# Kernel tuning notes

Hardware: AMD Instinct MI355X
Metric: run time of the kernel (lower is better)

Reference implementation:

```python
import jax, jax.numpy as jnp
import numpy as np
import math

C = 1.0                      # curvature (default in __call__)
SQRT_C = 1.0
MIN_ENORM = 1e-15
PROJ_EPS = 1e-5              # ball boundary margin for proj
CLAMPING_FACTOR = 1.0
SMOOTHING_FACTOR = 50.0
EPS32 = float(np.finfo(np.float32).eps)
CLAMP = CLAMPING_FACTOR * float(math.log(2.0 / EPS32))   # ~16.64


def proj(x, c=C):
    """Project points onto the Poincare ball of curvature c."""
    norm = jnp.linalg.norm(x, axis=-1, keepdims=True).clip(min=MIN_ENORM)
    max_norm = (1.0 - PROJ_EPS) / jnp.sqrt(c)
    return x * jnp.where(norm > max_norm, max_norm / norm, 1.0)


def conformal_factor(x, c=C):
    # lambda_x = 2 / (1 - c * ||x||^2), keepdims
    return 2.0 / (1.0 - c * jnp.sum(x * x, axis=-1, keepdims=True))


def smooth_clamp(x, lo, hi, s):
    """Smooth clamp via scaled softplus: -> clamp(x, lo, hi) as s -> inf."""
    sp = lambda z: jax.nn.softplus(s * z) / s
    return lo + sp(x - lo) - sp(x - hi)


def setup_inputs() -> dict:
    key = jax.random.key(0)
    k1, k2, k3 = jax.random.split(key, 3)
    B, D, P = 8192, 128, 128
    # manifold points: scale into the ball then project
    x = proj(0.1 * jax.random.normal(k1, (B, D), dtype=jnp.float32))
    weight = jax.random.normal(k2, (P, D), dtype=jnp.float32)
    bias = 0.01 * jax.random.normal(k3, (P, D), dtype=jnp.float32)
    return {"x": x, "weight": weight, "bias": bias}


def reference(x, weight, bias):
    c, sqrt_c = C, SQRT_C
    # 0) project bias onto manifold: (P, D)
    bias_PD = proj(bias, c)
    # 1) parallel transport weight from origin to bias: u * (lambda_0 / lambda_p) = u * (1 - c||p||^2)
    pt_weight_PD = weight * (1.0 - c * jnp.sum(bias_PD * bias_PD, axis=-1, keepdims=True))
    a = pt_weight_PD                 # (P, D)
    p_neg = -bias_PD                 # (P, D)
    # pairwise Mobius addition (-p) (+) x  -> (P, B, D)
    x2 = jnp.sum(x * x, axis=-1)                 # (B,)
    p2 = jnp.sum(p_neg * p_neg, axis=-1)         # (P,)
    dot = jnp.einsum("pd,bd->pb", p_neg, x)     # (P, B)
    coef_p = 1.0 + 2.0 * c * dot + c * x2[None, :]          # (P, B)
    coef_x = 1.0 - c * p2[:, None]                            # (P, 1)
    den = 1.0 + 2.0 * c * dot + (c * c) * p2[:, None] * x2[None, :]  # (P, B)
    sub_PBD = (coef_p[:, :, None] * p_neg[:, None, :] + coef_x[:, :, None] * x[None, :, :]) / den[:, :, None]
    sub_BPD = jnp.transpose(sub_PBD, (1, 0, 2))  # (B, P, D)
    # <sub, a> and norms
    suba_BP = jnp.einsum("bpd,pd->bp", sub_BPD, a)
    a_norm_P = jnp.linalg.norm(a, axis=-1).clip(min=MIN_ENORM)   # (P,)
    lambda_sub_BP = 2.0 / (1.0 - c * jnp.sum(sub_BPD * sub_BPD, axis=-1))  # (B, P)
    asinh_arg_BP = sqrt_c * lambda_sub_BP * suba_BP / a_norm_P[None, :]
    asinh_arg_BP = smooth_clamp(asinh_arg_BP, -CLAMP, CLAMP, SMOOTHING_FACTOR)
    signed_dist_BP = jnp.arcsinh(asinh_arg_BP) / sqrt_c
    lambda_p_P = 2.0 / (1.0 - c * jnp.sum(bias_PD * bias_PD, axis=-1))     # (P,)
    res_BP = lambda_p_P[None, :] * a_norm_P[None, :] * signed_dist_BP
    return res_BP
```

## Files before the change

### kernel.cpp

```cpp
#include <hip/hip_runtime.h>
#include <math.h>

namespace {
constexpr int Bn = 8192, Pn = 128, Dn = 128;
constexpr int BT = 64, PT = 32;
constexpr float MAXN = 1.0f - 1e-5f;
constexpr float CLAMPV = 16.63553233343869f;
constexpr float SMOOTH = 50.0f;
}

typedef short bf8 __attribute__((ext_vector_type(8)));
typedef float f32x4 __attribute__((ext_vector_type(4)));

__device__ __forceinline__ unsigned short bf16rn(float f) {
  unsigned int u = __float_as_uint(f);
  u = u + 0x7fffu + ((u >> 16) & 1u);
  return (unsigned short)(u >> 16);
}
__device__ __forceinline__ float bf2f(unsigned short h) {
  return __uint_as_float(((unsigned int)h) << 16);
}
__device__ __forceinline__ void split3(float f, unsigned short& h,
                                       unsigned short& m, unsigned short& l) {
  h = bf16rn(f); float r1 = f - bf2f(h);
  m = bf16rn(r1); float r2 = r1 - bf2f(m);
  l = bf16rn(r2);
}

__global__ __launch_bounds__(512, 4)
void fused_kernel(const float* __restrict__ x,
                  const float* __restrict__ weight,
                  const float* __restrict__ bias,
                  float* __restrict__ out) {
  __shared__ float4 lds4[4608];
  __shared__ double psum[96];
  __shared__ float x2A[64], fbA[64];
  __shared__ float bwA[32], iaA[32], soA[32];

  float* const scpf = reinterpret_cast<float*>(lds4 + 3072);
  float* const scxf = reinterpret_cast<float*>(lds4 + 3072 + 768);
  ushort4* const ldsu4 = reinterpret_cast<ushort4*>(lds4);
  const bf8* const ldsb = reinterpret_cast<const bf8*>(lds4);

  const int tid = threadIdx.x;
  const int b0 = blockIdx.x * BT;
  const int p0 = blockIdx.y * PT;
  const int rr = tid >> 5;
  const int cc = tid & 31;

  float4 xv[4], wv[2], bv[2];
#pragma unroll
  for (int q = 0; q < 4; ++q)
    xv[q] = *reinterpret_cast<const float4*>(x + (size_t)(b0 + 16 * q + rr) * Dn + cc * 4);
#pragma unroll
  for (int q = 0; q < 2; ++q) {
    wv[q] = *reinterpret_cast<const float4*>(weight + (size_t)(p0 + 16 * q + rr) * Dn + cc * 4);
    bv[q] = *reinterpret_cast<const float4*>(bias + (size_t)(p0 + 16 * q + rr) * Dn + cc * 4);
  }

#pragma unroll
  for (int q = 0; q < 4; ++q) {
    const int r = 16 * q + rr;
    float4 v = xv[q];
    float a[4] = {v.x, v.y, v.z, v.w};
    unsigned short h[4], m[4], lo[4];
#pragma unroll
    for (int e = 0; e < 4; ++e) split3(a[e], h[e], m[e], lo[e]);
    const int base = ((r * 16 + ((cc >> 1) ^ (r & 15))) << 1) + (cc & 1);
    ldsu4[base]            = make_ushort4(h[0], h[1], h[2], h[3]);
    ldsu4[2048 + base]     = make_ushort4(m[0], m[1], m[2], m[3]);
    ldsu4[4096 + base]     = make_ushort4(lo[0], lo[1], lo[2], lo[3]);
    scxf[q * 512 + tid] = fmaf(a[0], a[0], fmaf(a[1], a[1], fmaf(a[2], a[2], a[3] * a[3])));
  }
#pragma unroll
  for (int q = 0; q < 2; ++q) {
    float4 w = wv[q], b = bv[q];
    scpf[(q * 3 + 0) * 512 + tid] = fmaf(b.x, b.x, fmaf(b.y, b.y, fmaf(b.z, b.z, b.w * b.w)));
    scpf[(q * 3 + 1) * 512 + tid] = fmaf(b.x, w.x, fmaf(b.y, w.y, fmaf(b.z, w.z, b.w * w.w)));
    scpf[(q * 3 + 2) * 512 + tid] = fmaf(w.x, w.x, fmaf(w.y, w.y, fmaf(w.z, w.z, w.w * w.w)));
  }
  __syncthreads();

  if (tid < 96) {
    const int row = tid / 3;
    const int val = tid - 3 * row;
    const float4* base = reinterpret_cast<const float4*>(scpf) +
                         ((row >> 4) * 3 + val) * 128 + (row & 15) * 8;
    double s = 0.0;
#pragma unroll
    for (int jj = 0; jj < 8; ++jj) {
      float4 f = base[(jj + tid) & 7];
      s += (double)f.x + (double)f.y + (double)f.z + (double)f.w;
    }
    psum[tid] = s;
  } else if (tid >= 256 && tid < 320) {
    const int r = tid - 256;
    const float4* base = reinterpret_cast<const float4*>(scxf) +
                         (r >> 4) * 128 + (r & 15) * 8;
    double s = 0.0;
#pragma unroll
    for (int jj = 0; jj < 8; ++jj) {
      float4 f = base[(jj + tid) & 7];
      s += (double)f.x + (double)f.y + (double)f.z + (double)f.w;
    }
    x2A[r] = (float)s;
    fbA[r] = (float)(2.0 / (1.0 - s));
  }
  __syncthreads();

#pragma unroll
  for (int q = 0; q < 2; ++q) {
    const int r = 16 * q + rr;
    double nb2 = psum[3 * r + 0];
    double bwd = psum[3 * r + 1];
    double w2  = psum[3 * r + 2];
    double norm = sqrt(nb2);
    if (norm < 1e-15) norm = 1e-15;
    double scl = (norm > (double)MAXN) ? (double)MAXN / norm : 1.0;
    double p2 = nb2 * scl * scl;
    const float cxf = (float)(1.0 - p2);
    const float bwf = (float)(scl * bwd);
    const float k2f = 2.0f * bwf * (float)scl;
    float4 w = wv[q], b = bv[q];
    float vvv[4];
    vvv[0] = fmaf(cxf, w.x, k2f * b.x);
    vvv[1] = fmaf(cxf, w.y, k2f * b.y);
    vvv[2] = fmaf(cxf, w.z, k2f * b.z);
    vvv[3] = fmaf(cxf, w.w, k2f * b.w);
    unsigned short h[4], m[4], lo[4];
#pragma unroll
    for (int e = 0; e < 4; ++e) split3(vvv[e], h[e], m[e], lo[e]);
    const int base = ((3072 + r * 16 + ((cc >> 1) ^ (r & 15))) << 1) + (cc & 1);
    ldsu4[base]        = make_ushort4(h[0], h[1], h[2], h[3]);
    ldsu4[1024 + base] = make_ushort4(m[0], m[1], m[2], m[3]);
    ldsu4[2048 + base] = make_ushort4(lo[0], lo[1], lo[2], lo[3]);
    if (cc == 0) {
      float an = cxf * sqrtf((float)w2);
      if (an < 1e-15f) an = 1e-15f;
      bwA[r] = bwf;
      iaA[r] = 1.0f / an;
      soA[r] = 2.0f / cxf * an;
    }
  }
  __syncthreads();

  const int wid = tid >> 6;
  const int l = tid & 63;
  const int strip = wid & 3;
  const int khalf = wid >> 2;
  const int arow = strip * 16 + (l & 15);
  const int prow0 = l & 15, prow1 = 16 + (l & 15);
  const int kgrp = l >> 4;
  f32x4 acc0 = {0.f, 0.f, 0.f, 0.f}, acc1 = {0.f, 0.f, 0.f, 0.f};
#pragma unroll
  for (int kc2 = 0; kc2 < 2; ++kc2) {
    const int ga = ((khalf * 2 + kc2) * 4 + kgrp) ^ (l & 15);
    bf8 aH = ldsb[0 * 1024 + arow * 16 + ga];
    bf8 aM = ldsb[1 * 1024 + arow * 16 + ga];
    bf8 aL = ldsb[2 * 1024 + arow * 16 + ga];
    bf8 b0H = ldsb[3072 + 0 * 512 + prow0 * 16 + ga];
    bf8 b0M = ldsb[3072 + 1 * 512 + prow0 * 16 + ga];
    bf8 b0L = ldsb[3072 + 2 * 512 + prow0 * 16 + ga];
    bf8 b1H = ldsb[3072 + 0 * 512 + prow1 * 16 + ga];
    bf8 b1M = ldsb[3072 + 1 * 512 + prow1 * 16 + ga];
    bf8 b1L = ldsb[3072 + 2 * 512 + prow1 * 16 + ga];
    acc0 = __builtin_amdgcn_mfma_f32_16x16x32_bf16(aL, b0H, acc0, 0, 0, 0);
    acc0 = __builtin_amdgcn_mfma_f32_16x16x32_bf16(aH, b0L, acc0, 0, 0, 0);
    acc0 = __builtin_amdgcn_mfma_f32_16x16x32_bf16(aM, b0M, acc0, 0, 0, 0);
    acc0 = __builtin_amdgcn_mfma_f32_16x16x32_bf16(aM, b0H, acc0, 0, 0, 0);
    acc0 = __builtin_amdgcn_mfma_f32_16x16x32_bf16(aH, b0M, acc0, 0, 0, 0);
    acc0 = __builtin_amdgcn_mfma_f32_16x16x32_bf16(aH, b0H, acc0, 0, 0, 0);
    acc1 = __builtin_amdgcn_mfma_f32_16x16x32_bf16(aL, b1H, acc1, 0, 0, 0);
    acc1 = __builtin_amdgcn_mfma_f32_16x16x32_bf16(aH, b1L, acc1, 0, 0, 0);
    acc1 = __builtin_amdgcn_mfma_f32_16x16x32_bf16(aM, b1M, acc1, 0, 0, 0);
    acc1 = __builtin_amdgcn_mfma_f32_16x16x32_bf16(aM, b1H, acc1, 0, 0, 0);
    acc1 = __builtin_amdgcn_mfma_f32_16x16x32_bf16(aH, b1M, acc1, 0, 0, 0);
    acc1 = __builtin_amdgcn_mfma_f32_16x16x32_bf16(aH, b1H, acc1, 0, 0, 0);
  }
  __syncthreads();

  lds4[khalf * 512 + strip * 128 + 0 * 64 + l] =
      make_float4(acc0[0], acc0[1], acc0[2], acc0[3]);
  lds4[khalf * 512 + strip * 128 + 1 * 64 + l] =
      make_float4(acc1[0], acc1[1], acc1[2], acc1[3]);
  __syncthreads();

  {
    const int es = tid >> 7;
    const int et = (tid >> 6) & 1;
    const int el = tid & 63;
    float4 pa = lds4[es * 128 + et * 64 + el];
    float4 pb = lds4[512 + es * 128 + et * 64 + el];
    float s4[4] = {pa.x + pb.x, pa.y + pb.y, pa.z + pb.z, pa.w + pb.w};
    const int pl = et * 16 + (el & 15);
    const float bwp = bwA[pl], iap = iaA[pl], sop = soA[pl];
#pragma unroll
    for (int reg = 0; reg < 4; ++reg) {
      const int brl = es * 16 + (el >> 4) * 4 + reg;
      const float x2i = x2A[brl];
      const float fbi = fbA[brl];
      float X = fmaf(-(1.0f + x2i), bwp, s4[reg]);
      float arg = X * fbi * iap;
      float aa = fabsf(arg);
      float argc;
      if (aa <= CLAMPV - 0.35f) {
        argc = aa;
      } else if (aa >= CLAMPV + 0.35f) {
        argc = CLAMPV;
      } else {
        float z = SMOOTH * (aa - CLAMPV);
        float sp = (fmaxf(z, 0.0f) + log1pf(__expf(-fabsf(z)))) * (1.0f / SMOOTH);
        argc = aa - sp;
      }
      float r = __logf(argc + sqrtf(fmaf(argc, argc, 1.0f)));
      out[(size_t)(b0 + brl) * Pn + p0 + pl] = copysignf(sop * r, arg);
    }
  }
}

extern "C" void kernel_launch(void* const* d_in, const int* in_sizes, int n_in,
                              void* d_out, int out_size, void* d_ws, size_t ws_size,
                              hipStream_t stream) {
  const float* x = (const float*)d_in[0];
  const float* w = (const float*)d_in[1];
  const float* bias = (const float*)d_in[2];
  float* out = (float*)d_out;

  hipLaunchKernelGGL(fused_kernel, dim3(Bn / BT, Pn / PT), dim3(512), 0, stream,
                     x, w, bias, out);
}
```

Before: 14.08 us.

## Split MFMA work by output tile instead of K halves to drop LDS reduction

Each of the 8 waves now owns a distinct 16x16 output tile (4 B-strips by 2 P-tiles) and runs the full K=128 loop, rather than pairs of waves each covering half of K and then combining partial sums through LDS. This removes a barrier plus the LDS store/load round trip for the partial accumulators, and the epilogue reads results straight from registers. Global loads are also regrouped so each thread handles 16 x-elements or 8 w/b-elements and writes 16-byte bf16 vectors to LDS. Partial norms are reduced in float per thread before the double-precision sum, which slightly changes the numerics.

```diff
diff --git a/kernel.cpp b/kernel.cpp
--- a/kernel.cpp
+++ b/kernel.cpp
@@ -10,6 +10,7 @@
 }
 
 typedef short bf8 __attribute__((ext_vector_type(8)));
+typedef unsigned short u16x8 __attribute__((ext_vector_type(8)));
 typedef float f32x4 __attribute__((ext_vector_type(4)));
 
 __device__ __forceinline__ unsigned short bf16rn(float f) {
@@ -37,83 +38,89 @@
   __shared__ float x2A[64], fbA[64];
   __shared__ float bwA[32], iaA[32], soA[32];
 
-  float* const scpf = reinterpret_cast<float*>(lds4 + 3072);
-  float* const scxf = reinterpret_cast<float*>(lds4 + 3072 + 768);
-  ushort4* const ldsu4 = reinterpret_cast<ushort4*>(lds4);
-  const bf8* const ldsb = reinterpret_cast<const bf8*>(lds4);
+  u16x8* const LU = reinterpret_cast<u16x8*>(lds4);
+  const bf8* const LB = reinterpret_cast<const bf8*>(lds4);
+  float* const scp = reinterpret_cast<float*>(lds4 + 3072);
+  float* const scx = scp + 1536;
 
   const int tid = threadIdx.x;
   const int b0 = blockIdx.x * BT;
   const int p0 = blockIdx.y * PT;
-  const int rr = tid >> 5;
-  const int cc = tid & 31;
-
-  float4 xv[4], wv[2], bv[2];
-#pragma unroll
-  for (int q = 0; q < 4; ++q)
-    xv[q] = *reinterpret_cast<const float4*>(x + (size_t)(b0 + 16 * q + rr) * Dn + cc * 4);
-#pragma unroll
-  for (int q = 0; q < 2; ++q) {
-    wv[q] = *reinterpret_cast<const float4*>(weight + (size_t)(p0 + 16 * q + rr) * Dn + cc * 4);
-    bv[q] = *reinterpret_cast<const float4*>(bias + (size_t)(p0 + 16 * q + rr) * Dn + cc * 4);
-  }
-
-#pragma unroll
-  for (int q = 0; q < 4; ++q) {
-    const int r = 16 * q + rr;
-    float4 v = xv[q];
-    float a[4] = {v.x, v.y, v.z, v.w};
-    unsigned short h[4], m[4], lo[4];
-#pragma unroll
-    for (int e = 0; e < 4; ++e) split3(a[e], h[e], m[e], lo[e]);
-    const int base = ((r * 16 + ((cc >> 1) ^ (r & 15))) << 1) + (cc & 1);
-    ldsu4[base]            = make_ushort4(h[0], h[1], h[2], h[3]);
-    ldsu4[2048 + base]     = make_ushort4(m[0], m[1], m[2], m[3]);
-    ldsu4[4096 + base]     = make_ushort4(lo[0], lo[1], lo[2], lo[3]);
-    scxf[q * 512 + tid] = fmaf(a[0], a[0], fmaf(a[1], a[1], fmaf(a[2], a[2], a[3] * a[3])));
-  }
-#pragma unroll
-  for (int q = 0; q < 2; ++q) {
-    float4 w = wv[q], b = bv[q];
-    scpf[(q * 3 + 0) * 512 + tid] = fmaf(b.x, b.x, fmaf(b.y, b.y, fmaf(b.z, b.z, b.w * b.w)));
-    scpf[(q * 3 + 1) * 512 + tid] = fmaf(b.x, w.x, fmaf(b.y, w.y, fmaf(b.z, w.z, b.w * w.w)));
-    scpf[(q * 3 + 2) * 512 + tid] = fmaf(w.x, w.x, fmaf(w.y, w.y, fmaf(w.z, w.z, w.w * w.w)));
+
+  const int rA = tid >> 3, sA = tid & 7;
+  {
+    float xe[16];
+    const float* xr = x + (size_t)(b0 + rA) * Dn + sA * 16;
+#pragma unroll
+    for (int j = 0; j < 4; ++j) {
+      float4 q = *reinterpret_cast<const float4*>(xr + 4 * j);
+      xe[4 * j] = q.x; xe[4 * j + 1] = q.y; xe[4 * j + 2] = q.z; xe[4 * j + 3] = q.w;
+    }
+    float s2 = 0.f;
+#pragma unroll
+    for (int e = 0; e < 16; ++e) s2 = fmaf(xe[e], xe[e], s2);
+    scx[sA * 64 + rA] = s2;
+    const int sw = rA & 15;
+#pragma unroll
+    for (int g = 0; g < 2; ++g) {
+      u16x8 H, M, L;
+#pragma unroll
+      for (int e = 0; e < 8; ++e) {
+        unsigned short h, m, l;
+        split3(xe[g * 8 + e], h, m, l);
+        H[e] = h; M[e] = m; L[e] = l;
+      }
+      const int slot = rA * 16 + ((2 * sA + g) ^ sw);
+      LU[slot] = H;
+      LU[1024 + slot] = M;
+      LU[2048 + slot] = L;
+    }
+  }
+  const int rP = tid >> 4, sP = tid & 15;
+  float we[8], be[8];
+  {
+    const float* wr = weight + (size_t)(p0 + rP) * Dn + sP * 8;
+    const float* br = bias + (size_t)(p0 + rP) * Dn + sP * 8;
+#pragma unroll
+    for (int j = 0; j < 2; ++j) {
+      float4 qw = *reinterpret_cast<const float4*>(wr + 4 * j);
+      float4 qb = *reinterpret_cast<const float4*>(br + 4 * j);
+      we[4 * j] = qw.x; we[4 * j + 1] = qw.y; we[4 * j + 2] = qw.z; we[4 * j + 3] = qw.w;
+      be[4 * j] = qb.x; be[4 * j + 1] = qb.y; be[4 * j + 2] = qb.z; be[4 * j + 3] = qb.w;
+    }
+    float nb2 = 0.f, bwd = 0.f, w2 = 0.f;
+#pragma unroll
+    for (int e = 0; e < 8; ++e) {
+      nb2 = fmaf(be[e], be[e], nb2);
+      bwd = fmaf(be[e], we[e], bwd);
+      w2  = fmaf(we[e], we[e], w2);
+    }
+    scp[0 * 512 + sP * 32 + rP] = nb2;
+    scp[1 * 512 + sP * 32 + rP] = bwd;
+    scp[2 * 512 + sP * 32 + rP] = w2;
   }
   __syncthreads();
 
   if (tid < 96) {
-    const int row = tid / 3;
-    const int val = tid - 3 * row;
-    const float4* base = reinterpret_cast<const float4*>(scpf) +
-                         ((row >> 4) * 3 + val) * 128 + (row & 15) * 8;
+    const int stat = tid >> 5, row = tid & 31;
     double s = 0.0;
 #pragma unroll
-    for (int jj = 0; jj < 8; ++jj) {
-      float4 f = base[(jj + tid) & 7];
-      s += (double)f.x + (double)f.y + (double)f.z + (double)f.w;
-    }
-    psum[tid] = s;
-  } else if (tid >= 256 && tid < 320) {
-    const int r = tid - 256;
-    const float4* base = reinterpret_cast<const float4*>(scxf) +
-                         (r >> 4) * 128 + (r & 15) * 8;
+    for (int j = 0; j < 16; ++j) s += (double)scp[stat * 512 + j * 32 + row];
+    psum[stat * 32 + row] = s;
+  } else if (tid >= 128 && tid < 192) {
+    const int r = tid - 128;
     double s = 0.0;
 #pragma unroll
-    for (int jj = 0; jj < 8; ++jj) {
-      float4 f = base[(jj + tid) & 7];
-      s += (double)f.x + (double)f.y + (double)f.z + (double)f.w;
-    }
+    for (int j = 0; j < 8; ++j) s += (double)scx[j * 64 + r];
     x2A[r] = (float)s;
     fbA[r] = (float)(2.0 / (1.0 - s));
   }
   __syncthreads();
 
-#pragma unroll
-  for (int q = 0; q < 2; ++q) {
-    const int r = 16 * q + rr;
-    double nb2 = psum[3 * r + 0];
-    double bwd = psum[3 * r + 1];
-    double w2  = psum[3 * r + 2];
+  {
+    double nb2 = psum[rP];
+    double bwd = psum[32 + rP];
+    double w2  = psum[64 + rP];
     double norm = sqrt(nb2);
     if (norm < 1e-15) norm = 1e-15;
     double scl = (norm > (double)MAXN) ? (double)MAXN / norm : 1.0;
@@ -121,85 +128,61 @@
     const float cxf = (float)(1.0 - p2);
     const float bwf = (float)(scl * bwd);
     const float k2f = 2.0f * bwf * (float)scl;
-    float4 w = wv[q], b = bv[q];
-    float vvv[4];
-    vvv[0] = fmaf(cxf, w.x, k2f * b.x);
-    vvv[1] = fmaf(cxf, w.y, k2f * b.y);
-    vvv[2] = fmaf(cxf, w.z, k2f * b.z);
-    vvv[3] = fmaf(cxf, w.w, k2f * b.w);
-    unsigned short h[4], m[4], lo[4];
-#pragma unroll
-    for (int e = 0; e < 4; ++e) split3(vvv[e], h[e], m[e], lo[e]);
-    const int base = ((3072 + r * 16 + ((cc >> 1) ^ (r & 15))) << 1) + (cc & 1);
-    ldsu4[base]        = make_ushort4(h[0], h[1], h[2], h[3]);
-    ldsu4[1024 + base] = make_ushort4(m[0], m[1], m[2], m[3]);
-    ldsu4[2048 + base] = make_ushort4(lo[0], lo[1], lo[2], lo[3]);
-    if (cc == 0) {
+    u16x8 VH, VM, VL;
+#pragma unroll
+    for (int e = 0; e < 8; ++e) {
+      float v = fmaf(cxf, we[e], k2f * be[e]);
+      unsigned short h, m, l;
+      split3(v, h, m, l);
+      VH[e] = h; VM[e] = m; VL[e] = l;
+    }
+    const int slot = 3072 + rP * 16 + (sP ^ (rP & 15));
+    LU[slot] = VH;
+    LU[512 + slot] = VM;
+    LU[1024 + slot] = VL;
+    if (sP == 0) {
       float an = cxf * sqrtf((float)w2);
       if (an < 1e-15f) an = 1e-15f;
-      bwA[r] = bwf;
-      iaA[r] = 1.0f / an;
-      soA[r] = 2.0f / cxf * an;
+      bwA[rP] = bwf;
+      iaA[rP] = 1.0f / an;
+      soA[rP] = 2.0f / cxf * an;
     }
   }
   __syncthreads();
 
-  const int wid = tid >> 6;
-  const int l = tid & 63;
-  const int strip = wid & 3;
-  const int khalf = wid >> 2;
-  const int arow = strip * 16 + (l & 15);
-  const int prow0 = l & 15, prow1 = 16 + (l & 15);
-  const int kgrp = l >> 4;
-  f32x4 acc0 = {0.f, 0.f, 0.f, 0.f}, acc1 = {0.f, 0.f, 0.f, 0.f};
-#pragma unroll
-  for (int kc2 = 0; kc2 < 2; ++kc2) {
-    const int ga = ((khalf * 2 + kc2) * 4 + kgrp) ^ (l & 15);
-    bf8 aH = ldsb[0 * 1024 + arow * 16 + ga];
-    bf8 aM = ldsb[1 * 1024 + arow * 16 + ga];
-    bf8 aL = ldsb[2 * 1024 + arow * 16 + ga];
-    bf8 b0H = ldsb[3072 + 0 * 512 + prow0 * 16 + ga];
-    bf8 b0M = ldsb[3072 + 1 * 512 + prow0 * 16 + ga];
-    bf8 b0L = ldsb[3072 + 2 * 512 + prow0 * 16 + ga];
-    bf8 b1H = ldsb[3072 + 0 * 512 + prow1 * 16 + ga];
-    bf8 b1M = ldsb[3072 + 1 * 512 + prow1 * 16 + ga];
-    bf8 b1L = ldsb[3072 + 2 * 512 + prow1 * 16 + ga];
-    acc0 = __builtin_amdgcn_mfma_f32_16x16x32_bf16(aL, b0H, acc0, 0, 0, 0);
-    acc0 = __builtin_amdgcn_mfma_f32_16x16x32_bf16(aH, b0L, acc0, 0, 0, 0);
-    acc0 = __builtin_amdgcn_mfma_f32_16x16x32_bf16(aM, b0M, acc0, 0, 0, 0);
-    acc0 = __builtin_amdgcn_mfma_f32_16x16x32_bf16(aM, b0H, acc0, 0, 0, 0);
-    acc0 = __builtin_amdgcn_mfma_f32_16x16x32_bf16(aH, b0M, acc0, 0, 0, 0);
-    acc0 = __builtin_amdgcn_mfma_f32_16x16x32_bf16(aH, b0H, acc0, 0, 0, 0);
-    acc1 = __builtin_amdgcn_mfma_f32_16x16x32_bf16(aL, b1H, acc1, 0, 0, 0);
-    acc1 = __builtin_amdgcn_mfma_f32_16x16x32_bf16(aH, b1L, acc1, 0, 0, 0);
-    acc1 = __builtin_amdgcn_mfma_f32_16x16x32_bf16(aM, b1M, acc1, 0, 0, 0);
-    acc1 = __builtin_amdgcn_mfma_f32_16x16x32_bf16(aM, b1H, acc1, 0, 0, 0);
-    acc1 = __builtin_amdgcn_mfma_f32_16x16x32_bf16(aH, b1M, acc1, 0, 0, 0);
-    acc1 = __builtin_amdgcn_mfma_f32_16x16x32_bf16(aH, b1H, acc1, 0, 0, 0);
-  }
-  __syncthreads();
-
-  lds4[khalf * 512 + strip * 128 + 0 * 64 + l] =
-      make_float4(acc0[0], acc0[1], acc0[2], acc0[3]);
-  lds4[khalf * 512 + strip * 128 + 1 * 64 + l] =
-      make_float4(acc1[0], acc1[1], acc1[2], acc1[3]);
-  __syncthreads();
-
-  {
-    const int es = tid >> 7;
-    const int et = (tid >> 6) & 1;
-    const int el = tid & 63;
-    float4 pa = lds4[es * 128 + et * 64 + el];
-    float4 pb = lds4[512 + es * 128 + et * 64 + el];
-    float s4[4] = {pa.x + pb.x, pa.y + pb.y, pa.z + pb.z, pa.w + pb.w};
-    const int pl = et * 16 + (el & 15);
+  const int wid = tid >> 6, l = tid & 63;
+  const int strip = wid & 3, ptile = wid >> 2;
+  const int l15 = l & 15;
+  const int arow = strip * 16 + l15;
+  const int prow = ptile * 16 + l15;
+  const int kg = l >> 4;
+  f32x4 acc = {0.f, 0.f, 0.f, 0.f};
+#pragma unroll
+  for (int kc = 0; kc < 4; ++kc) {
+    const int ga = (kc * 4 + kg) ^ l15;
+    bf8 aH = LB[arow * 16 + ga];
+    bf8 aM = LB[1024 + arow * 16 + ga];
+    bf8 aL = LB[2048 + arow * 16 + ga];
+    bf8 vH = LB[3072 + prow * 16 + ga];
+    bf8 vM = LB[3584 + prow * 16 + ga];
+    bf8 vL = LB[4096 + prow * 16 + ga];
+    acc = __builtin_amdgcn_mfma_f32_16x16x32_bf16(aL, vH, acc, 0, 0, 0);
+    acc = __builtin_amdgcn_mfma_f32_16x16x32_bf16(aH, vL, acc, 0, 0, 0);
+    acc = __builtin_amdgcn_mfma_f32_16x16x32_bf16(aM, vM, acc, 0, 0, 0);
+    acc = __builtin_amdgcn_mfma_f32_16x16x32_bf16(aM, vH, acc, 0, 0, 0);
+    acc = __builtin_amdgcn_mfma_f32_16x16x32_bf16(aH, vM, acc, 0, 0, 0);
+    acc = __builtin_amdgcn_mfma_f32_16x16x32_bf16(aH, vH, acc, 0, 0, 0);
+  }
+
+  {
+    const int pl = ptile * 16 + l15;
     const float bwp = bwA[pl], iap = iaA[pl], sop = soA[pl];
 #pragma unroll
     for (int reg = 0; reg < 4; ++reg) {
-      const int brl = es * 16 + (el >> 4) * 4 + reg;
+      const int brl = strip * 16 + (l >> 4) * 4 + reg;
       const float x2i = x2A[brl];
       const float fbi = fbA[brl];
-      float X = fmaf(-(1.0f + x2i), bwp, s4[reg]);
+      float X = fmaf(-(1.0f + x2i), bwp, acc[reg]);
       float arg = X * fbi * iap;
       float aa = fabsf(arg);
       float argc;
```

Result: faster. 13.05 us (-7.3%).
